# Kernel optimization log

Measured on AMD Instinct MI355X. Metric: run time of the kernel, lower is better.

The kernel has to match this reference:

```python
import jax, jax.numpy as jnp
import numpy as np
from jax import lax

HEADS = 8

def rotate_every_two(x):
    x1 = x[..., ::2]
    x2 = x[..., 1::2]
    return jnp.stack([-x2, x1], axis=-1).reshape(x.shape)

def theta_shift(x, sin, cos):
    # x: (b,n,N,d); sin/cos: (N,d) broadcast over b,n
    return x * cos + rotate_every_two(x) * sin

def setup_inputs() -> dict:
    key = jax.random.key(0)
    ks = jax.random.split(key, 8)
    B, C, H, W = 8, 256, 64, 64
    hd = C // HEADS
    return {
        'x': jax.random.normal(ks[0], (B, C, H, W), jnp.float32),
        'sin': jax.random.normal(ks[1], (H * W, hd), jnp.float32),
        'cos': jax.random.normal(ks[2], (H * W, hd), jnp.float32),
        'w_qkvo': jax.random.normal(ks[3], (4 * C, C), jnp.float32) * 0.02,
        'b_qkvo': jnp.zeros((4 * C,), jnp.float32),
        'w_lepe': jax.random.normal(ks[4], (C, 1, 5, 5), jnp.float32) * 0.02,
        'b_lepe': jnp.zeros((C,), jnp.float32),
        'w_proj': jax.random.normal(ks[5], (C, C), jnp.float32) * 0.02,
        'b_proj': jnp.zeros((C,), jnp.float32),
    }

def reference(x, sin, cos, w_qkvo, b_qkvo, w_lepe, b_lepe, w_proj, b_proj):
    B, C, H, W = x.shape
    heads = HEADS
    hd = C // heads
    N = H * W
    scale = hd ** (-0.5)

    # 1x1 conv qkvo
    qkvo = jnp.einsum('bchw,oc->bohw', x, w_qkvo) + b_qkvo[None, :, None, None]
    qkv = qkvo[:, :3 * C]
    o = qkvo[:, 3 * C:]

    # depthwise 5x5 lepe on v channels
    v_img = qkv[:, 2 * C:]
    lepe = lax.conv_general_dilated(
        v_img, w_lepe, (1, 1), [(2, 2), (2, 2)],
        dimension_numbers=('NCHW', 'OIHW', 'NCHW'),
        feature_group_count=C) + b_lepe[None, :, None, None]

    # b (m n d) h w -> m b n (h w) d
    qkv_r = qkv.reshape(B, 3, heads, hd, N).transpose(1, 0, 2, 4, 3)
    q, k, v = qkv_r[0], qkv_r[1], qkv_r[2]  # (b,n,N,d)

    q = jax.nn.elu(q) + 1.0
    k = jax.nn.elu(k) + 1.0

    # z = q @ mean_k^T * scale -> (b,n,N,1)
    z = jnp.einsum('bnld,bnd->bnl', q, k.mean(axis=2))[..., None] * scale

    q = theta_shift(q, sin, cos)
    k = theta_shift(k, sin, cos)

    s = (scale / N) ** 0.5
    kv = jnp.einsum('bnld,bnle->bnde', k * s, v * s)  # (b,n,d,d)
    v_mean = v.mean(axis=2, keepdims=True)  # (b,n,1,d)

    res = jnp.einsum('bnld,bnde->bnle', q, kv) * (1.0 + 1.0 / (z + 1e-6)) - z * v_mean

    # b n (h w) d -> b (n d) h w
    res = res.transpose(0, 1, 3, 2).reshape(B, C, H, W)
    res = res + lepe

    out = jnp.einsum('bchw,oc->bohw', res * o, w_proj) + b_proj[None, :, None, None]
    return out
```

## Files before the change

kernel.cpp:

```cpp
#include <hip/hip_runtime.h>
#include <hip/hip_bf16.h>

typedef unsigned short u16;
typedef unsigned int u32;
typedef short bf16x8 __attribute__((ext_vector_type(8)));
typedef float f32x4 __attribute__((ext_vector_type(4)));
typedef u32 u32x4 __attribute__((ext_vector_type(4)));

#define N_TOK 4096
#define C_DIM 256
#define HEADS 8
#define HD 32
#define SCALE_F 0.17677669529663687f

__device__ inline u16 f2bf(float f) {
    u32 u = __float_as_uint(f);
    u += 0x7fffu + ((u >> 16) & 1u);
    return (u16)(u >> 16);
}
__device__ inline float b2f(u16 h) { return __uint_as_float((u32)h << 16); }
__device__ inline float bf_lo(u32 u) { return __uint_as_float(u << 16); }
__device__ inline float bf_hi(u32 u) { return __uint_as_float(u & 0xffff0000u); }

__device__ inline void gload16(const void* g, void* l) {
    __builtin_amdgcn_global_load_lds((const __attribute__((address_space(1))) u32*)g,
                                     (__attribute__((address_space(3))) u32*)l, 16, 0, 0);
}

__device__ inline void store_out(float* p, float v) { *p = v; }
__device__ inline void store_out(u16* p, float v) { *p = f2bf(v); }

__global__ __launch_bounds__(256) void conv_w(const float* __restrict__ w1, const float* __restrict__ w2,
                                              u16* __restrict__ o1, u16* __restrict__ o2) {
    int i = blockIdx.x * 256 + threadIdx.x;
    if (i < 1024 * 256) o1[i] = f2bf(w1[i]);
    if (i < 256 * 256)  o2[i] = f2bf(w2[i]);
}

__global__ __launch_bounds__(256) void make_sc(const float* __restrict__ s, const float* __restrict__ c,
                                               u32* __restrict__ scT) {
    int l0 = blockIdx.x * 64;
    __shared__ float ts[64][33];
    __shared__ float tc[64][33];
    int t = threadIdx.x;
    int d = t & 31, r = t >> 5;
#pragma unroll
    for (int i = 0; i < 8; ++i) {
        ts[r + i * 8][d] = s[(size_t)(l0 + r + i * 8) * HD + d];
        tc[r + i * 8][d] = c[(size_t)(l0 + r + i * 8) * HD + d];
    }
    __syncthreads();
    int li = t & 63, dr = t >> 6;
#pragma unroll
    for (int i = 0; i < 8; ++i) {
        int dd = dr * 8 + i;
        scT[(size_t)dd * N_TOK + l0 + li] = (u32)f2bf(ts[li][dd]) | ((u32)f2bf(tc[li][dd]) << 16);
    }
}

__global__ __launch_bounds__(256) void transpose_x(const float* __restrict__ x, u16* __restrict__ xT) {
    int b = blockIdx.z;
    int c0 = blockIdx.y * 32, l0 = blockIdx.x * 32;
    const float* xb = x + ((size_t)b * C_DIM + c0) * N_TOK + l0;
    __shared__ u16 tl[32][33];
    int t = threadIdx.x;
    int li = t & 31, ci = t >> 5;
#pragma unroll
    for (int i = 0; i < 4; ++i)
        tl[ci + i * 8][li] = f2bf(xb[(size_t)(ci + i * 8) * N_TOK + li]);
    __syncthreads();
    int c2 = t & 15, lr = t >> 4;
    u16* outp = xT + ((size_t)b * N_TOK + l0) * C_DIM + c0;
#pragma unroll
    for (int i = 0; i < 2; ++i) {
        int l = lr + i * 16;
        u32 pv = (u32)tl[2 * c2][l] | ((u32)tl[2 * c2 + 1][l] << 16);
        *(u32*)(outp + (size_t)l * C_DIM + 2 * c2) = pv;
    }
}

template <typename TO>
__global__ __launch_bounds__(256) void gemm_bt(const u16* __restrict__ A, const u16* __restrict__ Bm,
                                               const float* __restrict__ bias, TO* __restrict__ C,
                                               int M, int L, int K) {
    int bt = blockIdx.z;
    int m0 = blockIdx.y * 128;
    int l0 = blockIdx.x * 128;
    const u16* Bb = Bm + (size_t)bt * L * K;
    TO* Cb = C + (size_t)bt * M * L;

    __shared__ u16 smem[17408];
    u16* As = smem;
    u16* Bs = smem + 8192;
    u16* Cs = smem;

    int t = threadIdx.x;
    int w = t >> 6, lane = t & 63;
    int wr = (w >> 1) * 64, wc = (w & 1) * 64;
    int fr = lane & 15, kg = lane >> 4;

    f32x4 acc[4][4] = {};

    for (int k0 = 0; k0 < K; k0 += 64) {
#pragma unroll
        for (int j = 0; j < 4; ++j) {
            int c = j * 256 + w * 64 + lane;
            int row = c >> 3, slot = c & 7;
            int gslot = slot ^ (row & 7);
            u16* abase = As + (size_t)(j * 256 + w * 64) * 8;
            u16* bbase = Bs + (size_t)(j * 256 + w * 64) * 8;
            gload16(A + (size_t)(m0 + row) * K + k0 + gslot * 8, abase);
            gload16(Bb + (size_t)(l0 + row) * K + k0 + gslot * 8, bbase);
        }
        __syncthreads();
#pragma unroll
        for (int kk = 0; kk < 2; ++kk) {
            bf16x8 af[4], bfr[4];
#pragma unroll
            for (int i = 0; i < 4; ++i) {
                int ra = wr + i * 16 + fr;
                int rb = wc + i * 16 + fr;
                af[i]  = *(const bf16x8*)(As + (size_t)ra * 64 + (size_t)((kk * 4 + kg) ^ (ra & 7)) * 8);
                bfr[i] = *(const bf16x8*)(Bs + (size_t)rb * 64 + (size_t)((kk * 4 + kg) ^ (rb & 7)) * 8);
            }
#pragma unroll
            for (int i = 0; i < 4; ++i)
#pragma unroll
                for (int jj = 0; jj < 4; ++jj)
                    acc[i][jj] = __builtin_amdgcn_mfma_f32_16x16x32_bf16(af[i], bfr[jj], acc[i][jj], 0, 0, 0);
        }
        __syncthreads();
    }

    int rg = (lane >> 4) * 4;
    if constexpr (sizeof(TO) == 2) {
#pragma unroll
        for (int i = 0; i < 4; ++i)
#pragma unroll
            for (int jj = 0; jj < 4; ++jj) {
                int col = wc + jj * 16 + fr;
#pragma unroll
                for (int r = 0; r < 4; ++r) {
                    int row = wr + i * 16 + rg + r;
                    Cs[row * 136 + col] = f2bf(acc[i][jj][r] + bias[m0 + row]);
                }
            }
        __syncthreads();
        u16* CbT = (u16*)Cb;
#pragma unroll
        for (int j = 0; j < 8; ++j) {
            int id = j * 256 + t;
            int row = id >> 4, c8 = (id & 15) * 8;
            *(uint4*)(CbT + (size_t)(m0 + row) * L + l0 + c8) = *(const uint4*)(Cs + row * 136 + c8);
        }
    } else {
#pragma unroll
        for (int i = 0; i < 4; ++i)
#pragma unroll
            for (int jj = 0; jj < 4; ++jj) {
                int col = l0 + wc + jj * 16 + fr;
#pragma unroll
                for (int r = 0; r < 4; ++r) {
                    int row = m0 + wr + i * 16 + rg + r;
                    store_out(Cb + (size_t)row * L + col, acc[i][jj][r] + bias[row]);
                }
            }
    }
}

__global__ __launch_bounds__(256) void lepe_conv(const u16* __restrict__ qkvo, const float* __restrict__ wl,
                                                 const float* __restrict__ bl, u16* __restrict__ lepe) {
    int c = blockIdx.x, b = blockIdx.y;
    const u16* src = qkvo + ((size_t)b * 1024 + 512 + c) * N_TOK;
    u16* dst = lepe + ((size_t)b * C_DIM + c) * N_TOK;
    __shared__ float wc5[25];
    int t = threadIdx.x;
    if (t < 25) wc5[t] = wl[c * 25 + t];
    __syncthreads();

    int h = t >> 2, w0 = (t & 3) * 16;
    float bb = bl[c];
    float o16[16];
#pragma unroll
    for (int i = 0; i < 16; ++i) o16[i] = bb;

#pragma unroll
    for (int dh = 0; dh < 5; ++dh) {
        int gr = h + dh - 2;
        bool rowok = (gr >= 0) && (gr < 64);
        const u16* rp = src + (size_t)(rowok ? gr : 0) * 64 + w0 - 8;
        bf16x8 L0 = ((const bf16x8*)rp)[0];
        bf16x8 L1 = ((const bf16x8*)rp)[1];
        bf16x8 L2 = ((const bf16x8*)rp)[2];
        bf16x8 L3 = ((const bf16x8*)rp)[3];
        float rbuf[32];
#pragma unroll
        for (int j = 0; j < 32; ++j) {
            int col = w0 - 8 + j;
            u16 raw = (u16)(j < 8 ? L0[j] : j < 16 ? L1[j - 8] : j < 24 ? L2[j - 16] : L3[j - 24]);
            bool ok = rowok && (col >= 0) && (col < 64);
            rbuf[j] = ok ? b2f(raw) : 0.f;
        }
#pragma unroll
        for (int dw = 0; dw < 5; ++dw) {
            float wv_ = wc5[dh * 5 + dw];
#pragma unroll
            for (int ow = 0; ow < 16; ++ow)
                o16[ow] += rbuf[6 + dw + ow] * wv_;
        }
    }

    uint4 u0, u1;
    u0.x = (u32)f2bf(o16[0]) | ((u32)f2bf(o16[1]) << 16);
    u0.y = (u32)f2bf(o16[2]) | ((u32)f2bf(o16[3]) << 16);
    u0.z = (u32)f2bf(o16[4]) | ((u32)f2bf(o16[5]) << 16);
    u0.w = (u32)f2bf(o16[6]) | ((u32)f2bf(o16[7]) << 16);
    u1.x = (u32)f2bf(o16[8]) | ((u32)f2bf(o16[9]) << 16);
    u1.y = (u32)f2bf(o16[10]) | ((u32)f2bf(o16[11]) << 16);
    u1.z = (u32)f2bf(o16[12]) | ((u32)f2bf(o16[13]) << 16);
    u1.w = (u32)f2bf(o16[14]) | ((u32)f2bf(o16[15]) << 16);
    *(uint4*)(dst + h * 64 + w0) = u0;
    *(uint4*)(dst + h * 64 + w0 + 8) = u1;
}

__global__ __launch_bounds__(256) void kv_reduce(const u16* __restrict__ qkvo, const u32* __restrict__ scT,
                                                 float* __restrict__ part_kv, float* __restrict__ part_ks,
                                                 float* __restrict__ part_vs) {
    int chunk = blockIdx.x, bn = blockIdx.y;
    int b = bn >> 3, n = bn & 7;
    const u16* kp = qkvo + ((size_t)b * 1024 + 256 + n * HD) * N_TOK;
    const u16* vp = qkvo + ((size_t)b * 1024 + 512 + n * HD) * N_TOK;
    int lbase = chunk * 256;

    __shared__ u16 ks_bf[32][136];
    __shared__ u16 v_bf[32][136];
    __shared__ float red[4096];
    __shared__ float redk[32], redv[32];

    int t = threadIdx.x;
    int w = t >> 6, lane = t & 63;
    int fr = lane & 15, kg = lane >> 4;

    int p = t >> 4, g = t & 15;
    int dv = t >> 3, g2 = t & 7;

    f32x4 acc[2][2] = {};
    float ks0 = 0.f, ks1 = 0.f, vs = 0.f;

    for (int st = 0; st < 2; ++st) {
        int tok0 = lbase + st * 128;
        if (st) __syncthreads();
        const u16* k0p = kp + (size_t)(2 * p) * N_TOK + tok0 + g * 8;
        const u16* k1p = k0p + N_TOK;
        const u32* s0p = scT + (size_t)(2 * p) * N_TOK + tok0 + g * 8;
        const u32* s1p = s0p + N_TOK;
        bf16x8 k0 = *(const bf16x8*)k0p;
        bf16x8 k1 = *(const bf16x8*)k1p;
        u32x4 s0a = ((const u32x4*)s0p)[0], s0b = ((const u32x4*)s0p)[1];
        u32x4 s1a = ((const u32x4*)s1p)[0], s1b = ((const u32x4*)s1p)[1];
        const u16* vpp = vp + (size_t)dv * N_TOK + tok0 + g2 * 16;
        bf16x8 va = ((const bf16x8*)vpp)[0];
        bf16x8 vb = ((const bf16x8*)vpp)[1];

        u16 o0[8], o1[8];
#pragma unroll
        for (int j = 0; j < 8; ++j) {
            float kv0 = b2f((u16)k0[j]);
            float kv1 = b2f((u16)k1[j]);
            u32 sc0 = j < 4 ? s0a[j] : s0b[j - 4];
            u32 sc1 = j < 4 ? s1a[j] : s1b[j - 4];
            float e0 = kv0 > 0.f ? kv0 + 1.f : __expf(kv0);
            float e1 = kv1 > 0.f ? kv1 + 1.f : __expf(kv1);
            ks0 += e0; ks1 += e1;
            float se = bf_lo(sc0), ce = bf_hi(sc0);
            float so = bf_lo(sc1), co = bf_hi(sc1);
            o0[j] = f2bf(e0 * ce - e1 * se);
            o1[j] = f2bf(e1 * co + e0 * so);
        }
        u32x4 w0, w1;
#pragma unroll
        for (int q = 0; q < 4; ++q) {
            w0[q] = (u32)o0[2 * q] | ((u32)o0[2 * q + 1] << 16);
            w1[q] = (u32)o1[2 * q] | ((u32)o1[2 * q + 1] << 16);
        }
        *(u32x4*)&ks_bf[2 * p][g * 8] = w0;
        *(u32x4*)&ks_bf[2 * p + 1][g * 8] = w1;

#pragma unroll
        for (int j = 0; j < 8; ++j) { vs += b2f((u16)va[j]); }
#pragma unroll
        for (int j = 0; j < 8; ++j) { vs += b2f((u16)vb[j]); }
        *(bf16x8*)&v_bf[dv][g2 * 16] = va;
        *(bf16x8*)&v_bf[dv][g2 * 16 + 8] = vb;
        __syncthreads();

        int kcol = w * 32 + kg * 8;
        bf16x8 af[2], bfv[2];
#pragma unroll
        for (int i = 0; i < 2; ++i) {
            af[i]  = *(const bf16x8*)&ks_bf[i * 16 + fr][kcol];
            bfv[i] = *(const bf16x8*)&v_bf[i * 16 + fr][kcol];
        }
#pragma unroll
        for (int i = 0; i < 2; ++i)
#pragma unroll
            for (int jj = 0; jj < 2; ++jj)
                acc[i][jj] = __builtin_amdgcn_mfma_f32_16x16x32_bf16(af[i], bfv[jj], acc[i][jj], 0, 0, 0);
    }

#pragma unroll
    for (int i = 0; i < 2; ++i)
#pragma unroll
        for (int jj = 0; jj < 2; ++jj)
#pragma unroll
            for (int r = 0; r < 4; ++r) {
                int row = i * 16 + kg * 4 + r;
                int col = jj * 16 + fr;
                red[w * 1024 + row * 32 + col] = acc[i][jj][r];
            }

#pragma unroll
    for (int m = 1; m < 16; m <<= 1) {
        ks0 += __shfl_xor(ks0, m);
        ks1 += __shfl_xor(ks1, m);
    }
    if ((lane & 15) == 0) { redk[2 * p] = ks0; redk[2 * p + 1] = ks1; }
#pragma unroll
    for (int m = 1; m < 8; m <<= 1) vs += __shfl_xor(vs, m);
    if ((lane & 7) == 0) redv[dv] = vs;
    __syncthreads();

    float* pkv = part_kv + ((size_t)bn * 16 + chunk) * 1024;
#pragma unroll
    for (int i = 0; i < 4; ++i) {
        int el = i * 256 + t;
        pkv[el] = red[el] + red[1024 + el] + red[2048 + el] + red[3072 + el];
    }
    if (t < 32) {
        part_ks[((size_t)bn * 16 + chunk) * 32 + t] = redk[t];
        part_vs[((size_t)bn * 16 + chunk) * 32 + t] = redv[t];
    }
}

__global__ __launch_bounds__(256) void kv_final(const float* __restrict__ part_kv, const float* __restrict__ part_ks,
                                                const float* __restrict__ part_vs, u16* __restrict__ kvT_bf,
                                                float* __restrict__ kmean, float* __restrict__ vmean) {
    int bn = blockIdx.x;
    int t = threadIdx.x;
    const float* p = part_kv + (size_t)bn * 16 * 1024;
    const float s2c = SCALE_F / (float)N_TOK;
#pragma unroll
    for (int i = 0; i < 4; ++i) {
        int sl = t + i * 256;
        float s = 0;
#pragma unroll
        for (int c = 0; c < 16; ++c) s += p[(size_t)c * 1024 + sl];
        float val = s * s2c;
        int d = sl >> 5, e = sl & 31;
        kvT_bf[(size_t)bn * 1024 + e * 32 + d] = f2bf(val);
    }
    if (t < 32) {
        float s = 0, sv = 0;
        for (int c = 0; c < 16; ++c) {
            s  += part_ks[((size_t)bn * 16 + c) * 32 + t];
            sv += part_vs[((size_t)bn * 16 + c) * 32 + t];
        }
        kmean[bn * 32 + t] = s * (1.f / (float)N_TOK);
        vmean[bn * 32 + t] = sv * (1.f / (float)N_TOK);
    }
}

__global__ __launch_bounds__(256) void attn_epilogue(const u16* __restrict__ qkvo, const u32* __restrict__ scT,
                                                     const u16* __restrict__ kvT_bf, const float* __restrict__ kmean,
                                                     const float* __restrict__ vmean, const u16* __restrict__ lepe,
                                                     u16* __restrict__ resnT) {
    int lt = blockIdx.x, bn = blockIdx.y;
    int b = bn >> 3, n = bn & 7;
    const u16* qp = qkvo + ((size_t)b * 1024 + n * HD) * N_TOK;
    const u16* op = qkvo + ((size_t)b * 1024 + 768 + n * HD) * N_TOK;
    const u16* lp = lepe + ((size_t)b * C_DIM + n * HD) * N_TOK;

    __shared__ u16 kvb[32 * 40];
    __shared__ float kml[32], vml[32];
    __shared__ u16 Atile[4][64 * 40];
    __shared__ float Rtile[4][64 * 36];

    int t = threadIdx.x;
    int w = t >> 6, lane = t & 63;

    if (t < 128) {
        int e = t >> 2, d0 = (t & 3) * 8;
        *(uint4*)(kvb + e * 40 + d0) = *(const uint4*)(kvT_bf + (size_t)bn * 1024 + e * 32 + d0);
    }
    if (t < 32) { kml[t] = kmean[bn * 32 + t]; vml[t] = vmean[bn * 32 + t]; }
    __syncthreads();

    int token = lt * 256 + w * 64 + lane;

    float qv[32];
    float z = 0.f;
#pragma unroll
    for (int d = 0; d < 32; ++d) {
        float x_ = b2f(qp[(size_t)d * N_TOK + token]);
        float e_ = x_ > 0.f ? x_ + 1.f : __expf(x_);
        qv[d] = e_;
        z += e_ * kml[d];
    }
    z *= SCALE_F;
#pragma unroll
    for (int p = 0; p < 16; ++p) {
        u32 sc0 = scT[(size_t)(2 * p) * N_TOK + token];
        u32 sc1 = scT[(size_t)(2 * p + 1) * N_TOK + token];
        float se = bf_lo(sc0), ce = bf_hi(sc0);
        float so = bf_lo(sc1), co = bf_hi(sc1);
        float a = qv[2 * p], bb = qv[2 * p + 1];
        qv[2 * p]     = a * ce - bb * se;
        qv[2 * p + 1] = bb * co + a * so;
    }
    float mult = 1.f + 1.f / (z + 1e-6f);

    u16* Aw = Atile[w];
#pragma unroll
    for (int j4 = 0; j4 < 4; ++j4) {
        uint4 u;
        u.x = (u32)f2bf(qv[8 * j4 + 0]) | ((u32)f2bf(qv[8 * j4 + 1]) << 16);
        u.y = (u32)f2bf(qv[8 * j4 + 2]) | ((u32)f2bf(qv[8 * j4 + 3]) << 16);
        u.z = (u32)f2bf(qv[8 * j4 + 4]) | ((u32)f2bf(qv[8 * j4 + 5]) << 16);
        u.w = (u32)f2bf(qv[8 * j4 + 6]) | ((u32)f2bf(qv[8 * j4 + 7]) << 16);
        *(uint4*)(Aw + lane * 40 + j4 * 8) = u;
    }
    __syncthreads();

    int fr = lane & 15, kg = lane >> 4;
    bf16x8 af[4], bfr[2];
#pragma unroll
    for (int i = 0; i < 4; ++i)
        af[i] = *(const bf16x8*)(Aw + (i * 16 + fr) * 40 + kg * 8);
#pragma unroll
    for (int jj = 0; jj < 2; ++jj)
        bfr[jj] = *(const bf16x8*)(kvb + (jj * 16 + fr) * 40 + kg * 8);

    float* Rw = Rtile[w];
    f32x4 zero = {0.f, 0.f, 0.f, 0.f};
#pragma unroll
    for (int i = 0; i < 4; ++i)
#pragma unroll
        for (int jj = 0; jj < 2; ++jj) {
            f32x4 acc = __builtin_amdgcn_mfma_f32_16x16x32_bf16(af[i], bfr[jj], zero, 0, 0, 0);
#pragma unroll
            for (int r = 0; r < 4; ++r)
                Rw[(i * 16 + kg * 4 + r) * 36 + jj * 16 + fr] = acc[r];
        }
    __syncthreads();

    float res[32];
#pragma unroll
    for (int j = 0; j < 8; ++j) {
        f32x4 vr = *(const f32x4*)(Rw + lane * 36 + j * 4);
        res[4 * j] = vr[0]; res[4 * j + 1] = vr[1]; res[4 * j + 2] = vr[2]; res[4 * j + 3] = vr[3];
    }

    u16* dst0 = resnT + ((size_t)b * N_TOK + token) * C_DIM + n * HD;
#pragma unroll
    for (int g = 0; g < 4; ++g) {
        float vv[8];
#pragma unroll
        for (int e2 = 0; e2 < 8; ++e2) {
            int ee = g * 8 + e2;
            float lx = b2f(lp[(size_t)ee * N_TOK + token]);
            float ov = b2f(op[(size_t)ee * N_TOK + token]);
            float rx = res[ee] * mult - z * vml[ee];
            vv[e2] = (rx + lx) * ov;
        }
        uint4 u;
        u.x = (u32)f2bf(vv[0]) | ((u32)f2bf(vv[1]) << 16);
        u.y = (u32)f2bf(vv[2]) | ((u32)f2bf(vv[3]) << 16);
        u.z = (u32)f2bf(vv[4]) | ((u32)f2bf(vv[5]) << 16);
        u.w = (u32)f2bf(vv[6]) | ((u32)f2bf(vv[7]) << 16);
        ((uint4*)(dst0 + g * 8))[0] = u;
    }
}

extern "C" void kernel_launch(void* const* d_in, const int* in_sizes, int n_in,
                              void* d_out, int out_size, void* d_ws, size_t ws_size,
                              hipStream_t stream) {
    const float* x      = (const float*)d_in[0];
    const float* sinp   = (const float*)d_in[1];
    const float* cosp   = (const float*)d_in[2];
    const float* w_qkvo = (const float*)d_in[3];
    const float* b_qkvo = (const float*)d_in[4];
    const float* w_lepe = (const float*)d_in[5];
    const float* b_lepe = (const float*)d_in[6];
    const float* w_proj = (const float*)d_in[7];
    const float* b_proj = (const float*)d_in[8];

    char* ws = (char*)d_ws;
    size_t off = 0;
    auto alloc = [&](size_t bytes) { size_t o = off; off = (off + bytes + 255) & ~(size_t)255; return o; };
    u16*   wbf     = (u16*)(ws + alloc((size_t)1024 * 256 * 2));
    u16*   wpbf    = (u16*)(ws + alloc((size_t)256 * 256 * 2));
    u16*   xT      = (u16*)(ws + alloc((size_t)8 * 4096 * 256 * 2));
    u16*   qkvo    = (u16*)(ws + alloc((size_t)8 * 1024 * 4096 * 2));
    u16*   lepe    = (u16*)(ws + alloc((size_t)8 * 256 * 4096 * 2));
    u16*   resnT   = (u16*)(ws + alloc((size_t)8 * 4096 * 256 * 2));
    float* part_kv = (float*)(ws + alloc((size_t)64 * 16 * 1024 * 4));
    float* part_ks = (float*)(ws + alloc((size_t)64 * 16 * 32 * 4));
    float* part_vs = (float*)(ws + alloc((size_t)64 * 16 * 32 * 4));
    u16*   kvT_bf  = (u16*)(ws + alloc((size_t)64 * 1024 * 2));
    float* kmean   = (float*)(ws + alloc((size_t)64 * 32 * 4));
    float* vmean   = (float*)(ws + alloc((size_t)64 * 32 * 4));
    u32*   scT     = (u32*)(ws + alloc((size_t)32 * 4096 * 4));
    if (off > ws_size) return;

    conv_w<<<dim3(1024), dim3(256), 0, stream>>>(w_qkvo, w_proj, wbf, wpbf);
    make_sc<<<dim3(64), dim3(256), 0, stream>>>(sinp, cosp, scT);
    transpose_x<<<dim3(128, 8, 8), dim3(256), 0, stream>>>(x, xT);
    gemm_bt<u16><<<dim3(32, 8, 8), dim3(256), 0, stream>>>(wbf, xT, b_qkvo, qkvo, 1024, 4096, 256);
    lepe_conv<<<dim3(256, 8), dim3(256), 0, stream>>>(qkvo, w_lepe, b_lepe, lepe);
    kv_reduce<<<dim3(16, 64), dim3(256), 0, stream>>>(qkvo, scT, part_kv, part_ks, part_vs);
    kv_final<<<dim3(64), dim3(256), 0, stream>>>(part_kv, part_ks, part_vs, kvT_bf, kmean, vmean);
    attn_epilogue<<<dim3(16, 64), dim3(256), 0, stream>>>(qkvo, scT, kvT_bf, kmean, vmean, lepe, resnT);
    gemm_bt<float><<<dim3(32, 2, 8), dim3(256), 0, stream>>>(wpbf, resnT, b_proj, (float*)d_out, 256, 4096, 256);
}
```

Before: 112.0 us.

## Enlarge QKVO GEMM tile to 256x256 with 512 threads and merge prep kernels

Result: no change. 112.6 us (+0.6%).

```diff
diff --git a/kernel.cpp b/kernel.cpp
--- a/kernel.cpp
+++ b/kernel.cpp
@@ -27,22 +27,20 @@
                                      (__attribute__((address_space(3))) u32*)l, 16, 0, 0);
 }
 
-__device__ inline void store_out(float* p, float v) { *p = v; }
-__device__ inline void store_out(u16* p, float v) { *p = f2bf(v); }
-
-__global__ __launch_bounds__(256) void conv_w(const float* __restrict__ w1, const float* __restrict__ w2,
-                                              u16* __restrict__ o1, u16* __restrict__ o2) {
-    int i = blockIdx.x * 256 + threadIdx.x;
-    if (i < 1024 * 256) o1[i] = f2bf(w1[i]);
-    if (i < 256 * 256)  o2[i] = f2bf(w2[i]);
-}
-
-__global__ __launch_bounds__(256) void make_sc(const float* __restrict__ s, const float* __restrict__ c,
-                                               u32* __restrict__ scT) {
-    int l0 = blockIdx.x * 64;
+__global__ __launch_bounds__(256) void prep(const float* __restrict__ w1, const float* __restrict__ w2,
+                                            const float* __restrict__ s, const float* __restrict__ c,
+                                            u16* __restrict__ o1, u16* __restrict__ o2, u32* __restrict__ scT) {
+    int bx = blockIdx.x;
+    int t = threadIdx.x;
+    if (bx < 1024) {
+        int i = bx * 256 + t;
+        o1[i] = f2bf(w1[i]);
+        if (i < 256 * 256) o2[i] = f2bf(w2[i]);
+        return;
+    }
+    int l0 = (bx - 1024) * 64;
     __shared__ float ts[64][33];
     __shared__ float tc[64][33];
-    int t = threadIdx.x;
     int d = t & 31, r = t >> 5;
 #pragma unroll
     for (int i = 0; i < 8; ++i) {
@@ -79,20 +77,100 @@
     }
 }
 
-template <typename TO>
-__global__ __launch_bounds__(256) void gemm_bt(const u16* __restrict__ A, const u16* __restrict__ Bm,
-                                               const float* __restrict__ bias, TO* __restrict__ C,
-                                               int M, int L, int K) {
+__global__ __launch_bounds__(512) void gemm_qkvo(const u16* __restrict__ A, const u16* __restrict__ Bm,
+                                                 const float* __restrict__ bias, u16* __restrict__ C,
+                                                 int M, int L, int K) {
+    int bt = blockIdx.z;
+    int m0 = blockIdx.y * 256;
+    int l0 = blockIdx.x * 256;
+    const u16* Bb = Bm + (size_t)bt * L * K;
+    u16* Cb = C + (size_t)bt * M * L;
+
+    __shared__ u16 smem[34816];
+    u16* As = smem;
+    u16* Bs = smem + 16384;
+    u16* Cs = smem;
+
+    int t = threadIdx.x;
+    int w = t >> 6, lane = t & 63;
+    int wm = w >> 2, wl = w & 3;
+    int fr = lane & 15, kg = lane >> 4;
+
+    f32x4 acc[8][4] = {};
+
+    for (int k0 = 0; k0 < K; k0 += 64) {
+#pragma unroll
+        for (int j = 0; j < 4; ++j) {
+            int c = j * 512 + t;
+            int row = c >> 3, slot = c & 7;
+            int gslot = slot ^ (row & 7);
+            u16* abase = As + (size_t)(j * 512 + w * 64) * 8;
+            u16* bbase = Bs + (size_t)(j * 512 + w * 64) * 8;
+            gload16(A + (size_t)(m0 + row) * K + k0 + gslot * 8, abase);
+            gload16(Bb + (size_t)(l0 + row) * K + k0 + gslot * 8, bbase);
+        }
+        __syncthreads();
+#pragma unroll
+        for (int kk = 0; kk < 2; ++kk) {
+            bf16x8 af[8], bfr[4];
+#pragma unroll
+            for (int i = 0; i < 8; ++i) {
+                int ra = wm * 128 + i * 16 + fr;
+                af[i] = *(const bf16x8*)(As + (size_t)ra * 64 + (size_t)((kk * 4 + kg) ^ (ra & 7)) * 8);
+            }
+#pragma unroll
+            for (int jj = 0; jj < 4; ++jj) {
+                int rb = wl * 64 + jj * 16 + fr;
+                bfr[jj] = *(const bf16x8*)(Bs + (size_t)rb * 64 + (size_t)((kk * 4 + kg) ^ (rb & 7)) * 8);
+            }
+#pragma unroll
+            for (int i = 0; i < 8; ++i)
+#pragma unroll
+                for (int jj = 0; jj < 4; ++jj)
+                    acc[i][jj] = __builtin_amdgcn_mfma_f32_16x16x32_bf16(af[i], bfr[jj], acc[i][jj], 0, 0, 0);
+        }
+        __syncthreads();
+    }
+
+    int rg = kg * 4;
+#pragma unroll
+    for (int half = 0; half < 2; ++half) {
+        if (wm == half) {
+#pragma unroll
+            for (int i = 0; i < 8; ++i)
+#pragma unroll
+                for (int jj = 0; jj < 4; ++jj) {
+                    int col = wl * 64 + jj * 16 + fr;
+#pragma unroll
+                    for (int r = 0; r < 4; ++r) {
+                        int row = i * 16 + rg + r;
+                        Cs[row * 264 + col] = f2bf(acc[i][jj][r] + bias[m0 + half * 128 + row]);
+                    }
+                }
+        }
+        __syncthreads();
+#pragma unroll
+        for (int j = 0; j < 8; ++j) {
+            int id = j * 512 + t;
+            int row = id >> 5, c16 = (id & 31) * 8;
+            *(uint4*)(Cb + (size_t)(m0 + half * 128 + row) * L + l0 + c16) =
+                *(const uint4*)(Cs + row * 264 + c16);
+        }
+        __syncthreads();
+    }
+}
+
+__global__ __launch_bounds__(256) void gemm_bt_f32(const u16* __restrict__ A, const u16* __restrict__ Bm,
+                                                   const float* __restrict__ bias, float* __restrict__ C,
+                                                   int M, int L, int K) {
     int bt = blockIdx.z;
     int m0 = blockIdx.y * 128;
     int l0 = blockIdx.x * 128;
     const u16* Bb = Bm + (size_t)bt * L * K;
-    TO* Cb = C + (size_t)bt * M * L;
-
-    __shared__ u16 smem[17408];
-    u16* As = smem;
-    u16* Bs = smem + 8192;
-    u16* Cs = smem;
+    float* Cb = C + (size_t)bt * M * L;
+
+    __shared__ u16 As[128 * 64];
+    __shared__ u16 Bs[128 * 64];
 
     int t = threadIdx.x;
     int w = t >> 6, lane = t & 63;
@@ -133,39 +211,17 @@
     }
 
     int rg = (lane >> 4) * 4;
-    if constexpr (sizeof(TO) == 2) {
-#pragma unroll
-        for (int i = 0; i < 4; ++i)
-#pragma unroll
-            for (int jj = 0; jj < 4; ++jj) {
-                int col = wc + jj * 16 + fr;
-#pragma unroll
-                for (int r = 0; r < 4; ++r) {
-                    int row = wr + i * 16 + rg + r;
-                    Cs[row * 136 + col] = f2bf(acc[i][jj][r] + bias[m0 + row]);
-                }
+#pragma unroll
+    for (int i = 0; i < 4; ++i)
+#pragma unroll
+        for (int jj = 0; jj < 4; ++jj) {
+            int col = l0 + wc + jj * 16 + fr;
+#pragma unroll
+            for (int r = 0; r < 4; ++r) {
+                int row = m0 + wr + i * 16 + rg + r;
+                Cb[(size_t)row * L + col] = acc[i][jj][r] + bias[row];
             }
-        __syncthreads();
-        u16* CbT = (u16*)Cb;
-#pragma unroll
-        for (int j = 0; j < 8; ++j) {
-            int id = j * 256 + t;
-            int row = id >> 4, c8 = (id & 15) * 8;
-            *(uint4*)(CbT + (size_t)(m0 + row) * L + l0 + c8) = *(const uint4*)(Cs + row * 136 + c8);
-        }
-    } else {
-#pragma unroll
-        for (int i = 0; i < 4; ++i)
-#pragma unroll
-            for (int jj = 0; jj < 4; ++jj) {
-                int col = l0 + wc + jj * 16 + fr;
-#pragma unroll
-                for (int r = 0; r < 4; ++r) {
-                    int row = m0 + wr + i * 16 + rg + r;
-                    store_out(Cb + (size_t)row * L + col, acc[i][jj][r] + bias[row]);
-                }
-            }
-    }
+        }
 }
 
 __global__ __launch_bounds__(256) void lepe_conv(const u16* __restrict__ qkvo, const float* __restrict__ wl,
@@ -512,13 +568,12 @@
     u32*   scT     = (u32*)(ws + alloc((size_t)32 * 4096 * 4));
     if (off > ws_size) return;
 
-    conv_w<<<dim3(1024), dim3(256), 0, stream>>>(w_qkvo, w_proj, wbf, wpbf);
-    make_sc<<<dim3(64), dim3(256), 0, stream>>>(sinp, cosp, scT);
+    prep<<<dim3(1088), dim3(256), 0, stream>>>(w_qkvo, w_proj, sinp, cosp, wbf, wpbf, scT);
     transpose_x<<<dim3(128, 8, 8), dim3(256), 0, stream>>>(x, xT);
-    gemm_bt<u16><<<dim3(32, 8, 8), dim3(256), 0, stream>>>(wbf, xT, b_qkvo, qkvo, 1024, 4096, 256);
+    gemm_qkvo<<<dim3(16, 4, 8), dim3(512), 0, stream>>>(wbf, xT, b_qkvo, qkvo, 1024, 4096, 256);
     lepe_conv<<<dim3(256, 8), dim3(256), 0, stream>>>(qkvo, w_lepe, b_lepe, lepe);
     kv_reduce<<<dim3(16, 64), dim3(256), 0, stream>>>(qkvo, scT, part_kv, part_ks, part_vs);
     kv_final<<<dim3(64), dim3(256), 0, stream>>>(part_kv, part_ks, part_vs, kvT_bf, kmean, vmean);
     attn_epilogue<<<dim3(16, 64), dim3(256), 0, stream>>>(qkvo, scT, kvT_bf, kmean, vmean, lepe, resnT);
-    gemm_bt<float><<<dim3(32, 2, 8), dim3(256), 0, stream>>>(wpbf, resnT, b_proj, (float*)d_out, 256, 4096, 256);
-}
+    gemm_bt_f32<<<dim3(32, 2, 8), dim3(256), 0, stream>>>(wpbf, resnT, b_proj, (float*)d_out, 256, 4096, 256);
+}
```
